# Performance work log

Hardware: AMD Instinct MI355X
Metric: run time of the kernel (lower is better)

## Reference

```python
import jax, jax.numpy as jnp
from jax import lax
import numpy as np

B = 8192
NUM_CTX = 300; NUM_STN = 300; NUM_GPE = 20; NUM_GPI = 2; NUM_OUT = 20
FF_DIM = 20; FF_STEPS = 20; STN_ITERS = 50
ETA_GPE = 1.0; ETA_STN = 1.0 / 3.0; ETA_GPI = 0.1
A1 = 1.0; A2 = 1.0; THETAD1 = 0.0; THETAD2 = 0.0
UNITS = (64, 128, 64)

_SPECS = [("vf0", UNITS[0], NUM_CTX), ("vf1", UNITS[1], UNITS[0]), ("vf2", UNITS[2], UNITS[1]), ("vf3", 1, UNITS[2]),
          ("jd1", FF_DIM, NUM_CTX), ("jd2", FF_DIM, NUM_CTX), ("kd1", FF_DIM, NUM_CTX), ("kd2", FF_DIM, NUM_CTX),
          ("sg", NUM_GPE, NUM_STN), ("gs", NUM_STN, NUM_GPE), ("glat", NUM_GPE, NUM_GPE), ("slat", NUM_STN, NUM_STN),
          ("d1gpi", NUM_GPI, FF_DIM), ("stngpi", NUM_GPI, NUM_STN),
          ("ih", 4 * NUM_OUT, NUM_GPI), ("hh", 4 * NUM_OUT, NUM_OUT)]


def _lin_init(k, out_d, in_d):
    kw, kb = jax.random.split(k)
    bound = 1.0 / np.sqrt(in_d)
    w = jax.random.uniform(kw, (out_d, in_d), minval=-bound, maxval=bound, dtype=jnp.float32)
    b = jax.random.uniform(kb, (out_d,), minval=-bound, maxval=bound, dtype=jnp.float32)
    return w, b


def setup_inputs() -> dict:
    key = jax.random.key(0)
    ks = iter(jax.random.split(key, 40))
    inp = {}
    inp["stimulus"] = jax.random.normal(next(ks), (B, NUM_CTX), dtype=jnp.float32)
    inp["deltavf"] = jax.random.normal(next(ks), (B, 1), dtype=jnp.float32)
    inp["hx0"] = jax.random.uniform(next(ks), (B, NUM_OUT), dtype=jnp.float32)
    inp["cx0"] = jax.random.uniform(next(ks), (B, NUM_OUT), dtype=jnp.float32)
    for name, o, i in _SPECS:
        w, b = _lin_init(next(ks), o, i)
        inp["w_" + name] = w
        inp["b_" + name] = b
    return inp


def _lin(x, w, b):
    return x @ w.T + b


def _lstm_cell(x, h, c, w_ih, b_ih, w_hh, b_hh):
    gates = _lin(x, w_ih, b_ih) + _lin(h, w_hh, b_hh)
    i, f, g, o = jnp.split(gates, 4, axis=-1)  # torch LSTMCell gate order
    c_new = jax.nn.sigmoid(f) * c + jax.nn.sigmoid(i) * jnp.tanh(g)
    h_new = jax.nn.sigmoid(o) * jnp.tanh(c_new)
    return h_new, c_new


def reference(stimulus, deltavf, hx0, cx0,
              w_vf0, b_vf0, w_vf1, b_vf1, w_vf2, b_vf2, w_vf3, b_vf3,
              w_jd1, b_jd1, w_jd2, b_jd2, w_kd1, b_kd1, w_kd2, b_kd2,
              w_sg, b_sg, w_gs, b_gs, w_glat, b_glat, w_slat, b_slat,
              w_d1gpi, b_d1gpi, w_stngpi, b_stngpi,
              w_ih, b_ih, w_hh, b_hh):
    bsz = stimulus.shape[0]
    # value function head
    h = jax.nn.relu(_lin(stimulus, w_vf0, b_vf0))
    h = jax.nn.relu(_lin(h, w_vf1, b_vf1))
    h = jax.nn.relu(_lin(h, w_vf2, b_vf2))
    vt = jnp.tanh(_lin(h, w_vf3, b_vf3))  # [B, 1]

    lamd1 = jax.nn.sigmoid(A1 * (deltavf - THETAD1))  # [B, 1]
    lamd2 = jax.nn.sigmoid(A2 * (deltavf - THETAD2))  # [B, 1]

    # loop-invariant striatal drives (computed every iter in torch, same value)
    J_D1 = _lin(stimulus, w_jd1, b_jd1)
    J_D2 = _lin(stimulus, w_jd2, b_jd2)
    K_D1 = _lin(stimulus, w_kd1, b_kd1)
    K_D2 = _lin(stimulus, w_kd2, b_kd2)

    def ff_step(carry, _):
        v1, v2 = carry
        v1 = jax.nn.sigmoid(lamd1 * (J_D1 * (1.0 - v1) + (1.0 - K_D1) * v1))
        v2 = jax.nn.sigmoid(lamd2 * (J_D2 * (1.0 - v2) + (1.0 - K_D2) * v2))
        return (v1, v2), None

    z_ff = jnp.zeros((bsz, FF_DIM), dtype=stimulus.dtype)
    (V_D1, V_D2), _ = lax.scan(ff_step, (z_ff, z_ff), None, length=FF_STEPS)

    V_GPi_DP = _lin(V_D1, w_d1gpi, b_d1gpi)  # [B, num_gpi]

    def stn_step(carry, _):
        xgpe, xstn, vstn, vgpi, hx, cx = carry
        xgpe = xgpe + ETA_GPE * (-xgpe + _lin(vstn, w_sg, b_sg) + _lin(xgpe, w_glat, b_glat) - V_D2)
        xstn = xstn + ETA_STN * (-xstn + _lin(xgpe, w_gs, b_gs) + _lin(vstn, w_slat, b_slat))
        vstn = jnp.tanh(lamd2 * xstn)
        V_GPi_IP = lamd2 * _lin(vstn, w_stngpi, b_stngpi)
        vgpi = vgpi + ETA_GPI * (-vgpi - V_GPi_DP + 2.0 * V_GPi_IP)
        hx, cx = _lstm_cell(-vgpi, hx, cx, w_ih, b_ih, w_hh, b_hh)
        return (xgpe, xstn, vstn, vgpi, hx, cx), None

    carry0 = (jnp.zeros((bsz, NUM_GPE), dtype=stimulus.dtype),
              jnp.zeros((bsz, NUM_STN), dtype=stimulus.dtype),
              jnp.zeros((bsz, NUM_STN), dtype=stimulus.dtype),  # tanh(lamd2*0) = 0
              jnp.zeros((bsz, NUM_GPI), dtype=stimulus.dtype),
              hx0, cx0)
    carry, _ = lax.scan(stn_step, carry0, None, length=STN_ITERS)
    hx = carry[4]
    return hx, vt
```

## Files before the change

kernel.cpp:

```cpp
#include <hip/hip_runtime.h>


typedef _Float16 f16_t;
typedef _Float16 f16x8 __attribute__((ext_vector_type(8)));
typedef _Float16 f16x4 __attribute__((ext_vector_type(4)));
typedef float floatx4 __attribute__((ext_vector_type(4)));

#define BTOT 8192
#define BM   32
#define NTHR 512
#define NBLK 256
#define VSTR 328
#define XST  32

struct Params {
  const float *stimulus, *deltavf, *hx0, *cx0;
  const float *w_vf0, *b_vf0, *w_vf1, *b_vf1, *w_vf2, *b_vf2, *w_vf3, *b_vf3;
  const float *w_jd1, *b_jd1, *w_jd2, *b_jd2, *w_kd1, *b_kd1, *w_kd2, *b_kd2;
  const float *w_sg, *b_sg, *w_gs, *b_gs, *w_glat, *b_glat, *w_slat, *b_slat;
  const float *w_d1gpi, *b_d1gpi, *w_stngpi, *b_stngpi;
  const float *w_ih, *b_ih, *w_hh, *b_hh;
  float* out;
};

struct __align__(16) Smem {
  f16_t vstn[BM * VSTR];
  f16_t xgpe[2][BM * XST];
  f16_t hxf[BM * XST];
  f16_t wB2[21 * 512];
  f16_t wsp[10 * 512];
  f16_t whh[5 * 512];
  union { float h1f[BM * 128]; float scr[3200]; float gates[BM * 80]; } u;
  float h0f[BM * 64];
  float V_D2f[BM * 20];
  float bsumS[304];
  float bsg[20];
  float bihh[80], wih0[80], wih1[80];
  float DPs[BM * 2], vgpis[BM * 2], lamS[BM];
};

__device__ __forceinline__ float rcp_f(float x) { return __builtin_amdgcn_rcpf(x); }
__device__ __forceinline__ float sigm_fast(float x) { return rcp_f(1.f + __expf(-x)); }
__device__ __forceinline__ float tanh_fast(float x) { return 1.f - 2.f * rcp_f(1.f + __expf(2.f * x)); }

__device__ __forceinline__ f16x8 ldfrag(const float* row, int k0, int kmax, bool valid) {
  float4 z = make_float4(0.f, 0.f, 0.f, 0.f);
  int nv = valid ? (kmax - k0) : 0;
  float4 f0 = (nv >= 4) ? *(const float4*)(row + k0) : z;
  float4 f1 = (nv >= 8) ? *(const float4*)(row + k0 + 4) : z;
  f16x8 r;
  r[0] = (f16_t)f0.x; r[1] = (f16_t)f0.y; r[2] = (f16_t)f0.z; r[3] = (f16_t)f0.w;
  r[4] = (f16_t)f1.x; r[5] = (f16_t)f1.y; r[6] = (f16_t)f1.z; r[7] = (f16_t)f1.w;
  return r;
}

__global__ __launch_bounds__(NTHR, 2) void bg_main(Params P) {
  __shared__ Smem S;
  const int tid  = threadIdx.x;
  const int lane = tid & 63;
  const int wv   = tid >> 6;
  const int q    = lane >> 4;
  const int cl   = lane & 15;
  const int row0 = blockIdx.x * BM;
  const floatx4 zf = {0.f, 0.f, 0.f, 0.f};

  if (tid < BM) S.lamS[tid] = sigm_fast(P.deltavf[row0 + tid]);
  for (int i = tid; i < BM * 2; i += NTHR) S.vgpis[i] = 0.f;
  for (int i = tid; i < 2 * BM * XST; i += NTHR) ((f16_t*)S.xgpe)[i] = (f16_t)0.f;
  for (int i = tid; i < BM * XST; i += NTHR) {
    int m = i >> 5, j = i & 31;
    S.hxf[i] = (j < 20) ? (f16_t)P.hx0[row0 * 20 + m * 20 + j] : (f16_t)0.f;
  }
  for (int i = tid; i < BM * VSTR; i += NTHR) S.vstn[i] = (f16_t)0.f;
  for (int i = tid; i < 21 * 512; i += NTHR) {
    int t = i >> 9, l = (i >> 3) & 63, jj = i & 7;
    int c2 = l & 15, k = ((l >> 4) << 3) + jj;
    float v = 0.f;
    if (t < 19) { int n = t * 16 + c2; if (n < 300 && k < 20) v = P.w_gs[n * 20 + k]; }
    else        { int g = (t - 19) * 16 + c2; if (g < 20 && k < 20) v = P.w_glat[g * 20 + k]; }
    S.wB2[i] = (f16_t)v;
  }
  for (int i = tid; i < 10 * 512; i += NTHR) {
    int c = i >> 9, l = (i >> 3) & 63, jj = i & 7;
    int p = l & 15, k = c * 32 + ((l >> 4) << 3) + jj;
    float v = (p < 2 && k < 300) ? P.w_stngpi[p * 300 + k] : 0.f;
    S.wsp[i] = (f16_t)v;
  }
  for (int i = tid; i < 5 * 512; i += NTHR) {
    int t = i >> 9, l = (i >> 3) & 63, jj = i & 7;
    int g = t * 16 + (l & 15), k = ((l >> 4) << 3) + jj;
    S.whh[i] = (f16_t)((k < 20) ? P.w_hh[g * 20 + k] : 0.f);
  }
  for (int i = tid; i < 304; i += NTHR) S.bsumS[i] = (i < 300) ? (P.b_slat[i] + P.b_gs[i]) : 0.f;
  for (int i = tid; i < 20; i += NTHR)  S.bsg[i] = P.b_sg[i] + P.b_glat[i];
  for (int i = tid; i < 80; i += NTHR) {
    S.bihh[i] = P.b_ih[i] + P.b_hh[i];
    S.wih0[i] = P.w_ih[i * 2 + 0];
    S.wih1[i] = P.w_ih[i * 2 + 1];
  }

  {
    int o = tid & 63, mb = (tid >> 6) * 4;
    const float4* wr = (const float4*)(P.w_vf0 + o * 300);
    float bias = P.b_vf0[o], a[4];
#pragma unroll
    for (int u = 0; u < 4; ++u) a[u] = bias;
    for (int kq = 0; kq < 75; ++kq) {
      float4 w = wr[kq];
#pragma unroll
      for (int u = 0; u < 4; ++u) {
        float4 v = *(const float4*)(P.stimulus + (size_t)(row0 + mb + u) * 300 + kq * 4);
        a[u] = fmaf(v.x, w.x, a[u]); a[u] = fmaf(v.y, w.y, a[u]);
        a[u] = fmaf(v.z, w.z, a[u]); a[u] = fmaf(v.w, w.w, a[u]);
      }
    }
#pragma unroll
    for (int u = 0; u < 4; ++u) S.h0f[(mb + u) * 64 + o] = fmaxf(a[u], 0.f);
  }
  __syncthreads();
  {
    int o = tid & 127, mb = (tid >> 7) * 8;
    const float* wr = P.w_vf1 + o * 64;
    float bias = P.b_vf1[o], a[8];
#pragma unroll
    for (int u = 0; u < 8; ++u) a[u] = bias;
    for (int k = 0; k < 64; ++k) {
      float w = wr[k];
#pragma unroll
      for (int u = 0; u < 8; ++u) a[u] = fmaf(S.h0f[(mb + u) * 64 + k], w, a[u]);
    }
#pragma unroll
    for (int u = 0; u < 8; ++u) S.u.h1f[(mb + u) * 128 + o] = fmaxf(a[u], 0.f);
  }
  __syncthreads();
  {
    int o = tid & 63, mb = (tid >> 6) * 4;
    const float* wr = P.w_vf2 + o * 128;
    float bias = P.b_vf2[o], a[4];
#pragma unroll
    for (int u = 0; u < 4; ++u) a[u] = bias;
    for (int k = 0; k < 128; ++k) {
      float w = wr[k];
#pragma unroll
      for (int u = 0; u < 4; ++u) a[u] = fmaf(S.u.h1f[(mb + u) * 128 + k], w, a[u]);
    }
#pragma unroll
    for (int u = 0; u < 4; ++u) S.h0f[(mb + u) * 64 + o] = fmaxf(a[u], 0.f);
  }
  __syncthreads();
  {
    int oid = tid & 127, mb = (tid >> 7) * 8;
    if (oid < 80) {
      int which = oid / 20, o = oid - which * 20;
      const float *wp, *bp;
      if (which == 0)      { wp = P.w_jd1; bp = P.b_jd1; }
      else if (which == 1) { wp = P.w_jd2; bp = P.b_jd2; }
      else if (which == 2) { wp = P.w_kd1; bp = P.b_kd1; }
      else                 { wp = P.w_kd2; bp = P.b_kd2; }
      float bias = bp[o], a[8];
#pragma unroll
      for (int u = 0; u < 8; ++u) a[u] = bias;
      for (int kq = 0; kq < 75; ++kq) {
        float4 w = *(const float4*)(wp + o * 300 + kq * 4);
#pragma unroll
        for (int u = 0; u < 8; ++u) {
          float4 v = *(const float4*)(P.stimulus + (size_t)(row0 + mb + u) * 300 + kq * 4);
          a[u] = fmaf(v.x, w.x, a[u]); a[u] = fmaf(v.y, w.y, a[u]);
          a[u] = fmaf(v.z, w.z, a[u]); a[u] = fmaf(v.w, w.w, a[u]);
        }
      }
#pragma unroll
      for (int u = 0; u < 8; ++u) S.u.scr[which * 640 + (mb + u) * 20 + o] = a[u];
    }
    if (tid < BM) {
      float a = P.b_vf3[0];
      for (int k = 0; k < 64; ++k) a = fmaf(S.h0f[tid * 64 + k], P.w_vf3[k], a);
      P.out[(size_t)BTOT * 20 + row0 + tid] = tanh_fast(a);
    }
  }
  __syncthreads();
  for (int i = tid; i < BM * 20; i += NTHR) {
    int m = i / 20;
    float j1 = S.u.scr[i],        j2 = S.u.scr[640 + i];
    float k1 = S.u.scr[1280 + i], k2 = S.u.scr[1920 + i];
    float L = S.lamS[m], v1 = 0.f, v2 = 0.f;
    for (int s = 0; s < 20; ++s) {
      v1 = sigm_fast(L * (j1 * (1.f - v1) + (1.f - k1) * v1));
      v2 = sigm_fast(L * (j2 * (1.f - v2) + (1.f - k2) * v2));
    }
    S.u.scr[2560 + i] = v1;
    S.V_D2f[i] = v2;
  }
  __syncthreads();
  if (tid < BM * 2) {
    int m = tid >> 1, p2 = tid & 1;
    float a = P.b_d1gpi[p2];
    for (int o = 0; o < 20; ++o) a = fmaf(S.u.scr[2560 + m * 20 + o], P.w_d1gpi[p2 * 20 + o], a);
    S.DPs[tid] = a;
  }
  __syncthreads();

  f16x8 Ws[3][10];
#pragma unroll
  for (int j = 0; j < 3; ++j) {
    int t = wv + 8 * j;
    if (t < 19) {
      int n = t * 16 + cl;
#pragma unroll
      for (int c = 0; c < 10; ++c)
        Ws[j][c] = ldfrag(P.w_slat + (size_t)(n < 300 ? n : 0) * 300, c * 32 + q * 8, 300, n < 300);
    } else if (t < 21) {
      int g = (t - 19) * 16 + cl;
#pragma unroll
      for (int c = 0; c < 10; ++c)
        Ws[j][c] = ldfrag(P.w_sg + (size_t)(g < 20 ? g : 0) * 300, c * 32 + q * 8, 300, g < 20);
    } else {
      f16x8 z;
#pragma unroll
      for (int e = 0; e < 8; ++e) z[e] = (f16_t)0.f;
#pragma unroll
      for (int c = 0; c < 10; ++c) Ws[j][c] = z;
    }
  }
  const float lam0 = S.lamS[cl], lam1 = S.lamS[cl + 16];
  const float bstn0 = P.b_stngpi[0], bstn1 = P.b_stngpi[1];
  const int e0 = tid,        m0 = e0 / 20, j0 = e0 - m0 * 20;
  const int e1 = tid + NTHR, m1 = e1 / 20, j1 = e1 - m1 * 20;
  const bool hase1 = (tid < BM * 20 - NTHR);
  float cxr0 = P.cx0[row0 * 20 + e0], hxr0 = P.hx0[row0 * 20 + e0];
  float cxr1 = hase1 ? P.cx0[row0 * 20 + e1] : 0.f;
  float hxr1 = hase1 ? P.hx0[row0 * 20 + e1] : 0.f;

  float xs[3][2][4];
#pragma unroll
  for (int j = 0; j < 3; ++j)
#pragma unroll
    for (int mf = 0; mf < 2; ++mf)
#pragma unroll
      for (int r = 0; r < 4; ++r) xs[j][mf][r] = 0.f;

  for (int it = 0; it < 50; ++it) {
    const int po = it & 1, pn = po ^ 1;
    floatx4 acc[3][2];
#pragma unroll
    for (int j = 0; j < 3; ++j) { acc[j][0] = zf; acc[j][1] = zf; }

#pragma unroll
    for (int c = 0; c < 10; ++c) {
      f16x8 b0 = *(const f16x8*)&S.vstn[cl * VSTR + c * 32 + q * 8];
      f16x8 b1 = *(const f16x8*)&S.vstn[(16 + cl) * VSTR + c * 32 + q * 8];
#pragma unroll
      for (int j = 0; j < 3; ++j) {
        if (wv + 8 * j < 21) {
          acc[j][0] = __builtin_amdgcn_mfma_f32_16x16x32_f16(Ws[j][c], b0, acc[j][0], 0, 0, 0);
          acc[j][1] = __builtin_amdgcn_mfma_f32_16x16x32_f16(Ws[j][c], b1, acc[j][1], 0, 0, 0);
        }
      }
    }
    if (wv == 3 || wv == 4) {
      f16x8 Wg = *(const f16x8*)&S.wB2[(wv + 16) * 512 + lane * 8];
      f16x8 g0 = *(const f16x8*)&S.xgpe[po][cl * XST + q * 8];
      f16x8 g1 = *(const f16x8*)&S.xgpe[po][(16 + cl) * XST + q * 8];
      acc[2][0] = __builtin_amdgcn_mfma_f32_16x16x32_f16(Wg, g0, acc[2][0], 0, 0, 0);
      acc[2][1] = __builtin_amdgcn_mfma_f32_16x16x32_f16(Wg, g1, acc[2][1], 0, 0, 0);
      int g0i = (wv - 3) * 16 + q * 4;
      if (g0i < 20) {
        floatx4 bg4 = *(const floatx4*)&S.bsg[g0i];
#pragma unroll
        for (int mf = 0; mf < 2; ++mf) {
          int batch = cl + 16 * mf;
          floatx4 vd4 = *(const floatx4*)&S.V_D2f[batch * 20 + g0i];
          f16x4 pk;
#pragma unroll
          for (int r = 0; r < 4; ++r) pk[r] = (f16_t)(acc[2][mf][r] + bg4[r] - vd4[r]);
          *(f16x4*)&S.xgpe[pn][batch * XST + g0i] = pk;
        }
      }
    }
    __syncthreads();

    {
      f16x8 x0 = *(const f16x8*)&S.xgpe[pn][cl * XST + q * 8];
      f16x8 x1 = *(const f16x8*)&S.xgpe[pn][(16 + cl) * XST + q * 8];
#pragma unroll
      for (int j = 0; j < 3; ++j) {
        int t = wv + 8 * j;
        if (t < 19) {
          f16x8 Wg = *(const f16x8*)&S.wB2[t * 512 + lane * 8];
          acc[j][0] = __builtin_amdgcn_mfma_f32_16x16x32_f16(Wg, x0, acc[j][0], 0, 0, 0);
          acc[j][1] = __builtin_amdgcn_mfma_f32_16x16x32_f16(Wg, x1, acc[j][1], 0, 0, 0);
        }
      }
#pragma unroll
      for (int j = 0; j < 3; ++j) {
        int t = wv + 8 * j;
        if (t < 19) {
          int n0 = t * 16 + q * 4;
          if (!(t == 18 && q == 3)) {
            floatx4 bs4 = *(const floatx4*)&S.bsumS[n0];
#pragma unroll
            for (int mf = 0; mf < 2; ++mf) {
              float lm = mf ? lam1 : lam0;
              f16x4 pk;
#pragma unroll
              for (int r = 0; r < 4; ++r) {
                float xo = xs[j][mf][r];
                float xn = xo + (1.0f / 3.0f) * (acc[j][mf][r] + bs4[r] - xo);
                xs[j][mf][r] = xn;
                pk[r] = (f16_t)tanh_fast(lm * xn);
              }
              *(f16x4*)&S.vstn[(cl + 16 * mf) * VSTR + n0] = pk;
            }
          }
        }
      }
    }
    __syncthreads();

    if (wv == 5) {
      floatx4 ip0 = zf, ip1 = zf;
#pragma unroll
      for (int c = 0; c < 10; ++c) {
        f16x8 Wp = *(const f16x8*)&S.wsp[c * 512 + lane * 8];
        f16x8 b0 = *(const f16x8*)&S.vstn[cl * VSTR + c * 32 + q * 8];
        f16x8 b1 = *(const f16x8*)&S.vstn[(16 + cl) * VSTR + c * 32 + q * 8];
        ip0 = __builtin_amdgcn_mfma_f32_16x16x32_f16(Wp, b0, ip0, 0, 0, 0);
        ip1 = __builtin_amdgcn_mfma_f32_16x16x32_f16(Wp, b1, ip1, 0, 0, 0);
      }
      if (q == 0) {
#pragma unroll
        for (int mf = 0; mf < 2; ++mf) {
          int batch = cl + 16 * mf;
          float lm = mf ? lam1 : lam0;
#pragma unroll
          for (int p = 0; p < 2; ++p) {
            float raw = (mf ? ip1[p] : ip0[p]) + (p ? bstn1 : bstn0);
            float ipv = lm * raw;
            int idx = batch * 2 + p;
            float v = S.vgpis[idx];
            v = v + 0.1f * (-v - S.DPs[idx] + 2.f * ipv);
            S.vgpis[idx] = v;
          }
        }
      }
    } else if (wv < 5) {
      f16x8 Wh = *(const f16x8*)&S.whh[wv * 512 + lane * 8];
      f16x8 h0 = *(const f16x8*)&S.hxf[cl * XST + q * 8];
      f16x8 h1 = *(const f16x8*)&S.hxf[(16 + cl) * XST + q * 8];
      floatx4 gA = __builtin_amdgcn_mfma_f32_16x16x32_f16(Wh, h0, zf, 0, 0, 0);
      floatx4 gB = __builtin_amdgcn_mfma_f32_16x16x32_f16(Wh, h1, zf, 0, 0, 0);
      int gb = wv * 16 + q * 4;
      *(floatx4*)&S.u.gates[cl * 80 + gb] = gA;
      *(floatx4*)&S.u.gates[(cl + 16) * 80 + gb] = gB;
    }
    __syncthreads();

    {
      float v0 = S.vgpis[m0 * 2], v1 = S.vgpis[m0 * 2 + 1];
      float gi = S.u.gates[m0 * 80 + j0]      + S.bihh[j0]      - S.wih0[j0] * v0      - S.wih1[j0] * v1;
      float gf = S.u.gates[m0 * 80 + 20 + j0] + S.bihh[20 + j0] - S.wih0[20 + j0] * v0 - S.wih1[20 + j0] * v1;
      float gg = S.u.gates[m0 * 80 + 40 + j0] + S.bihh[40 + j0] - S.wih0[40 + j0] * v0 - S.wih1[40 + j0] * v1;
      float go = S.u.gates[m0 * 80 + 60 + j0] + S.bihh[60 + j0] - S.wih0[60 + j0] * v0 - S.wih1[60 + j0] * v1;
      float cn = sigm_fast(gf) * cxr0 + sigm_fast(gi) * tanh_fast(gg);
      cxr0 = cn;
      hxr0 = sigm_fast(go) * tanh_fast(cn);
      S.hxf[m0 * XST + j0] = (f16_t)hxr0;
    }
    if (hase1) {
      float v0 = S.vgpis[m1 * 2], v1 = S.vgpis[m1 * 2 + 1];
      float gi = S.u.gates[m1 * 80 + j1]      + S.bihh[j1]      - S.wih0[j1] * v0      - S.wih1[j1] * v1;
      float gf = S.u.gates[m1 * 80 + 20 + j1] + S.bihh[20 + j1] - S.wih0[20 + j1] * v0 - S.wih1[20 + j1] * v1;
      float gg = S.u.gates[m1 * 80 + 40 + j1] + S.bihh[40 + j1] - S.wih0[40 + j1] * v0 - S.wih1[40 + j1] * v1;
      float go = S.u.gates[m1 * 80 + 60 + j1] + S.bihh[60 + j1] - S.wih0[60 + j1] * v0 - S.wih1[60 + j1] * v1;
      float cn = sigm_fast(gf) * cxr1 + sigm_fast(gi) * tanh_fast(gg);
      cxr1 = cn;
      hxr1 = sigm_fast(go) * tanh_fast(cn);
      S.hxf[m1 * XST + j1] = (f16_t)hxr1;
    }
    __syncthreads();
  }

  P.out[(size_t)row0 * 20 + e0] = hxr0;
  if (hase1) P.out[(size_t)row0 * 20 + e1] = hxr1;
}

extern "C" void kernel_launch(void* const* d_in, const int* in_sizes, int n_in,
                              void* d_out, int out_size, void* d_ws, size_t ws_size,
                              hipStream_t stream) {
  (void)in_sizes; (void)n_in; (void)out_size; (void)d_ws; (void)ws_size;
  Params P;
  P.stimulus = (const float*)d_in[0];
  P.deltavf  = (const float*)d_in[1];
  P.hx0 = (const float*)d_in[2];
  P.cx0 = (const float*)d_in[3];
  P.w_vf0 = (const float*)d_in[4];  P.b_vf0 = (const float*)d_in[5];
  P.w_vf1 = (const float*)d_in[6];  P.b_vf1 = (const float*)d_in[7];
  P.w_vf2 = (const float*)d_in[8];  P.b_vf2 = (const float*)d_in[9];
  P.w_vf3 = (const float*)d_in[10]; P.b_vf3 = (const float*)d_in[11];
  P.w_jd1 = (const float*)d_in[12]; P.b_jd1 = (const float*)d_in[13];
  P.w_jd2 = (const float*)d_in[14]; P.b_jd2 = (const float*)d_in[15];
  P.w_kd1 = (const float*)d_in[16]; P.b_kd1 = (const float*)d_in[17];
  P.w_kd2 = (const float*)d_in[18]; P.b_kd2 = (const float*)d_in[19];
  P.w_sg  = (const float*)d_in[20]; P.b_sg  = (const float*)d_in[21];
  P.w_gs  = (const float*)d_in[22]; P.b_gs  = (const float*)d_in[23];
  P.w_glat= (const float*)d_in[24]; P.b_glat= (const float*)d_in[25];
  P.w_slat= (const float*)d_in[26]; P.b_slat= (const float*)d_in[27];
  P.w_d1gpi  = (const float*)d_in[28]; P.b_d1gpi  = (const float*)d_in[29];
  P.w_stngpi = (const float*)d_in[30]; P.b_stngpi = (const float*)d_in[31];
  P.w_ih = (const float*)d_in[32]; P.b_ih = (const float*)d_in[33];
  P.w_hh = (const float*)d_in[34]; P.b_hh = (const float*)d_in[35];
  P.out  = (float*)d_out;
  bg_main<<<NBLK, NTHR, 0, stream>>>(P);
}
```

Before: 410.5 us.

## Pipeline GPi/LSTM stage on dedicated wavefront, overlapping next STN iteration

Gives the STN/GPe matrix products to seven wavefronts and hands the GPi readout plus the LSTM update to wavefront 7. That wavefront processes iteration it-1 while the others compute iteration it, which removes two of the four barriers per iteration. The stngpi and hh weights now live in that wave's registers instead of shared memory, LSTM state moves to shared arrays, and the h1 activations are stored as fp16 to shrink shared memory. The risks are serialising the LSTM work on a single wave and the lower precision of the h1 activations.

```diff
diff --git a/kernel.cpp b/kernel.cpp
--- a/kernel.cpp
+++ b/kernel.cpp
@@ -28,11 +28,14 @@
   f16_t xgpe[2][BM * XST];
   f16_t hxf[BM * XST];
   f16_t wB2[21 * 512];
-  f16_t wsp[10 * 512];
-  f16_t whh[5 * 512];
-  union { float h1f[BM * 128]; float scr[3200]; float gates[BM * 80]; } u;
+  union {
+    f16_t h1f[BM * 128];
+    float scr[2560];
+    float gates[BM * 80];
+  } u;
   float h0f[BM * 64];
   float V_D2f[BM * 20];
+  float cxL[BM * 20], hxL[BM * 20];
   float bsumS[304];
   float bsg[20];
   float bihh[80], wih0[80], wih1[80];
@@ -66,12 +69,16 @@
 
   if (tid < BM) S.lamS[tid] = sigm_fast(P.deltavf[row0 + tid]);
   for (int i = tid; i < BM * 2; i += NTHR) S.vgpis[i] = 0.f;
+  for (int i = tid; i < BM * VSTR; i += NTHR) S.vstn[i] = (f16_t)0.f;
   for (int i = tid; i < 2 * BM * XST; i += NTHR) ((f16_t*)S.xgpe)[i] = (f16_t)0.f;
   for (int i = tid; i < BM * XST; i += NTHR) {
     int m = i >> 5, j = i & 31;
     S.hxf[i] = (j < 20) ? (f16_t)P.hx0[row0 * 20 + m * 20 + j] : (f16_t)0.f;
   }
-  for (int i = tid; i < BM * VSTR; i += NTHR) S.vstn[i] = (f16_t)0.f;
+  for (int i = tid; i < BM * 20; i += NTHR) {
+    S.cxL[i] = P.cx0[row0 * 20 + i];
+    S.hxL[i] = P.hx0[row0 * 20 + i];
+  }
   for (int i = tid; i < 21 * 512; i += NTHR) {
     int t = i >> 9, l = (i >> 3) & 63, jj = i & 7;
     int c2 = l & 15, k = ((l >> 4) << 3) + jj;
@@ -80,17 +87,6 @@
     else        { int g = (t - 19) * 16 + c2; if (g < 20 && k < 20) v = P.w_glat[g * 20 + k]; }
     S.wB2[i] = (f16_t)v;
   }
-  for (int i = tid; i < 10 * 512; i += NTHR) {
-    int c = i >> 9, l = (i >> 3) & 63, jj = i & 7;
-    int p = l & 15, k = c * 32 + ((l >> 4) << 3) + jj;
-    float v = (p < 2 && k < 300) ? P.w_stngpi[p * 300 + k] : 0.f;
-    S.wsp[i] = (f16_t)v;
-  }
-  for (int i = tid; i < 5 * 512; i += NTHR) {
-    int t = i >> 9, l = (i >> 3) & 63, jj = i & 7;
-    int g = t * 16 + (l & 15), k = ((l >> 4) << 3) + jj;
-    S.whh[i] = (f16_t)((k < 20) ? P.w_hh[g * 20 + k] : 0.f);
-  }
   for (int i = tid; i < 304; i += NTHR) S.bsumS[i] = (i < 300) ? (P.b_slat[i] + P.b_gs[i]) : 0.f;
   for (int i = tid; i < 20; i += NTHR)  S.bsg[i] = P.b_sg[i] + P.b_glat[i];
   for (int i = tid; i < 80; i += NTHR) {
@@ -104,18 +100,18 @@
     const float4* wr = (const float4*)(P.w_vf0 + o * 300);
     float bias = P.b_vf0[o], a[4];
 #pragma unroll
-    for (int u = 0; u < 4; ++u) a[u] = bias;
+    for (int u2 = 0; u2 < 4; ++u2) a[u2] = bias;
     for (int kq = 0; kq < 75; ++kq) {
       float4 w = wr[kq];
 #pragma unroll
-      for (int u = 0; u < 4; ++u) {
-        float4 v = *(const float4*)(P.stimulus + (size_t)(row0 + mb + u) * 300 + kq * 4);
-        a[u] = fmaf(v.x, w.x, a[u]); a[u] = fmaf(v.y, w.y, a[u]);
-        a[u] = fmaf(v.z, w.z, a[u]); a[u] = fmaf(v.w, w.w, a[u]);
-      }
-    }
-#pragma unroll
-    for (int u = 0; u < 4; ++u) S.h0f[(mb + u) * 64 + o] = fmaxf(a[u], 0.f);
+      for (int u2 = 0; u2 < 4; ++u2) {
+        float4 v = *(const float4*)(P.stimulus + (size_t)(row0 + mb + u2) * 300 + kq * 4);
+        a[u2] = fmaf(v.x, w.x, a[u2]); a[u2] = fmaf(v.y, w.y, a[u2]);
+        a[u2] = fmaf(v.z, w.z, a[u2]); a[u2] = fmaf(v.w, w.w, a[u2]);
+      }
+    }
+#pragma unroll
+    for (int u2 = 0; u2 < 4; ++u2) S.h0f[(mb + u2) * 64 + o] = fmaxf(a[u2], 0.f);
   }
   __syncthreads();
   {
@@ -123,14 +119,14 @@
     const float* wr = P.w_vf1 + o * 64;
     float bias = P.b_vf1[o], a[8];
 #pragma unroll
-    for (int u = 0; u < 8; ++u) a[u] = bias;
+    for (int u2 = 0; u2 < 8; ++u2) a[u2] = bias;
     for (int k = 0; k < 64; ++k) {
       float w = wr[k];
 #pragma unroll
-      for (int u = 0; u < 8; ++u) a[u] = fmaf(S.h0f[(mb + u) * 64 + k], w, a[u]);
-    }
-#pragma unroll
-    for (int u = 0; u < 8; ++u) S.u.h1f[(mb + u) * 128 + o] = fmaxf(a[u], 0.f);
+      for (int u2 = 0; u2 < 8; ++u2) a[u2] = fmaf(S.h0f[(mb + u2) * 64 + k], w, a[u2]);
+    }
+#pragma unroll
+    for (int u2 = 0; u2 < 8; ++u2) S.u.h1f[(mb + u2) * 128 + o] = (f16_t)fmaxf(a[u2], 0.f);
   }
   __syncthreads();
   {
@@ -138,14 +134,14 @@
     const float* wr = P.w_vf2 + o * 128;
     float bias = P.b_vf2[o], a[4];
 #pragma unroll
-    for (int u = 0; u < 4; ++u) a[u] = bias;
+    for (int u2 = 0; u2 < 4; ++u2) a[u2] = bias;
     for (int k = 0; k < 128; ++k) {
       float w = wr[k];
 #pragma unroll
-      for (int u = 0; u < 4; ++u) a[u] = fmaf(S.u.h1f[(mb + u) * 128 + k], w, a[u]);
-    }
-#pragma unroll
-    for (int u = 0; u < 4; ++u) S.h0f[(mb + u) * 64 + o] = fmaxf(a[u], 0.f);
+      for (int u2 = 0; u2 < 4; ++u2) a[u2] = fmaf((float)S.u.h1f[(mb + u2) * 128 + k], w, a[u2]);
+    }
+#pragma unroll
+    for (int u2 = 0; u2 < 4; ++u2) S.h0f[(mb + u2) * 64 + o] = fmaxf(a[u2], 0.f);
   }
   __syncthreads();
   {
@@ -159,18 +155,18 @@
       else                 { wp = P.w_kd2; bp = P.b_kd2; }
       float bias = bp[o], a[8];
 #pragma unroll
-      for (int u = 0; u < 8; ++u) a[u] = bias;
+      for (int u2 = 0; u2 < 8; ++u2) a[u2] = bias;
       for (int kq = 0; kq < 75; ++kq) {
         float4 w = *(const float4*)(wp + o * 300 + kq * 4);
 #pragma unroll
-        for (int u = 0; u < 8; ++u) {
-          float4 v = *(const float4*)(P.stimulus + (size_t)(row0 + mb + u) * 300 + kq * 4);
-          a[u] = fmaf(v.x, w.x, a[u]); a[u] = fmaf(v.y, w.y, a[u]);
-          a[u] = fmaf(v.z, w.z, a[u]); a[u] = fmaf(v.w, w.w, a[u]);
+        for (int u2 = 0; u2 < 8; ++u2) {
+          float4 v = *(const float4*)(P.stimulus + (size_t)(row0 + mb + u2) * 300 + kq * 4);
+          a[u2] = fmaf(v.x, w.x, a[u2]); a[u2] = fmaf(v.y, w.y, a[u2]);
+          a[u2] = fmaf(v.z, w.z, a[u2]); a[u2] = fmaf(v.w, w.w, a[u2]);
         }
       }
 #pragma unroll
-      for (int u = 0; u < 8; ++u) S.u.scr[which * 640 + (mb + u) * 20 + o] = a[u];
+      for (int u2 = 0; u2 < 8; ++u2) S.u.scr[which * 640 + (mb + u2) * 20 + o] = a[u2];
     }
     if (tid < BM) {
       float a = P.b_vf3[0];
@@ -188,48 +184,47 @@
       v1 = sigm_fast(L * (j1 * (1.f - v1) + (1.f - k1) * v1));
       v2 = sigm_fast(L * (j2 * (1.f - v2) + (1.f - k2) * v2));
     }
-    S.u.scr[2560 + i] = v1;
     S.V_D2f[i] = v2;
+    S.h0f[i] = v1;
   }
   __syncthreads();
   if (tid < BM * 2) {
     int m = tid >> 1, p2 = tid & 1;
     float a = P.b_d1gpi[p2];
-    for (int o = 0; o < 20; ++o) a = fmaf(S.u.scr[2560 + m * 20 + o], P.w_d1gpi[p2 * 20 + o], a);
+    for (int o = 0; o < 20; ++o) a = fmaf(S.h0f[m * 20 + o], P.w_d1gpi[p2 * 20 + o], a);
     S.DPs[tid] = a;
   }
   __syncthreads();
 
   f16x8 Ws[3][10];
-#pragma unroll
-  for (int j = 0; j < 3; ++j) {
-    int t = wv + 8 * j;
-    if (t < 19) {
-      int n = t * 16 + cl;
-#pragma unroll
-      for (int c = 0; c < 10; ++c)
-        Ws[j][c] = ldfrag(P.w_slat + (size_t)(n < 300 ? n : 0) * 300, c * 32 + q * 8, 300, n < 300);
-    } else if (t < 21) {
-      int g = (t - 19) * 16 + cl;
-#pragma unroll
-      for (int c = 0; c < 10; ++c)
-        Ws[j][c] = ldfrag(P.w_sg + (size_t)(g < 20 ? g : 0) * 300, c * 32 + q * 8, 300, g < 20);
-    } else {
-      f16x8 z;
-#pragma unroll
-      for (int e = 0; e < 8; ++e) z[e] = (f16_t)0.f;
-#pragma unroll
-      for (int c = 0; c < 10; ++c) Ws[j][c] = z;
-    }
-  }
-  const float lam0 = S.lamS[cl], lam1 = S.lamS[cl + 16];
-  const float bstn0 = P.b_stngpi[0], bstn1 = P.b_stngpi[1];
-  const int e0 = tid,        m0 = e0 / 20, j0 = e0 - m0 * 20;
-  const int e1 = tid + NTHR, m1 = e1 / 20, j1 = e1 - m1 * 20;
-  const bool hase1 = (tid < BM * 20 - NTHR);
-  float cxr0 = P.cx0[row0 * 20 + e0], hxr0 = P.hx0[row0 * 20 + e0];
-  float cxr1 = hase1 ? P.cx0[row0 * 20 + e1] : 0.f;
-  float hxr1 = hase1 ? P.hx0[row0 * 20 + e1] : 0.f;
+  if (wv < 7) {
+#pragma unroll
+    for (int j = 0; j < 3; ++j) {
+      int t = wv + 7 * j;
+      if (t < 19) {
+        int n = t * 16 + cl;
+#pragma unroll
+        for (int c = 0; c < 10; ++c)
+          Ws[j][c] = ldfrag(P.w_slat + (size_t)(n < 300 ? n : 0) * 300, c * 32 + q * 8, 300, n < 300);
+      } else {
+        int g = (t - 19) * 16 + cl;
+#pragma unroll
+        for (int c = 0; c < 10; ++c)
+          Ws[j][c] = ldfrag(P.w_sg + (size_t)(g < 20 ? g : 0) * 300, c * 32 + q * 8, 300, g < 20);
+      }
+    }
+  }
+  f16x8 Wsp[10], Whh[5];
+  float bstn0 = 0.f, bstn1 = 0.f;
+  if (wv == 7) {
+#pragma unroll
+    for (int c = 0; c < 10; ++c)
+      Wsp[c] = ldfrag(P.w_stngpi + (size_t)(cl < 2 ? cl : 0) * 300, c * 32 + q * 8, 300, cl < 2);
+#pragma unroll
+    for (int gt = 0; gt < 5; ++gt)
+      Whh[gt] = ldfrag(P.w_hh + (size_t)(gt * 16 + cl) * 20, q * 8, 20, true);
+    bstn0 = P.b_stngpi[0]; bstn1 = P.b_stngpi[1];
+  }
 
   float xs[3][2][4];
 #pragma unroll
@@ -238,6 +233,68 @@
     for (int mf = 0; mf < 2; ++mf)
 #pragma unroll
       for (int r = 0; r < 4; ++r) xs[j][mf][r] = 0.f;
+
+  const int cm = lane >> 1, cj0 = (lane & 1) * 10;
+
+  auto consume = [&]() {
+    floatx4 ip0 = zf, ip1 = zf;
+#pragma unroll
+    for (int c = 0; c < 10; ++c) {
+      f16x8 b0 = *(const f16x8*)&S.vstn[cl * VSTR + c * 32 + q * 8];
+      f16x8 b1 = *(const f16x8*)&S.vstn[(16 + cl) * VSTR + c * 32 + q * 8];
+      ip0 = __builtin_amdgcn_mfma_f32_16x16x32_f16(Wsp[c], b0, ip0, 0, 0, 0);
+      ip1 = __builtin_amdgcn_mfma_f32_16x16x32_f16(Wsp[c], b1, ip1, 0, 0, 0);
+    }
+    if (q == 0) {
+#pragma unroll
+      for (int mf = 0; mf < 2; ++mf) {
+        int batch = cl + 16 * mf;
+        float lm = S.lamS[batch];
+#pragma unroll
+        for (int p = 0; p < 2; ++p) {
+          float raw = (mf ? ip1[p] : ip0[p]) + (p ? bstn1 : bstn0);
+          int idx = batch * 2 + p;
+          float v = S.vgpis[idx];
+          v = v + 0.1f * (-v - S.DPs[idx] + 2.f * (lm * raw));
+          S.vgpis[idx] = v;
+        }
+      }
+    }
+    f16x8 h0 = *(const f16x8*)&S.hxf[cl * XST + q * 8];
+    f16x8 h1 = *(const f16x8*)&S.hxf[(16 + cl) * XST + q * 8];
+    float vA0 = S.vgpis[cl * 2], vA1 = S.vgpis[cl * 2 + 1];
+    float vB0 = S.vgpis[(cl + 16) * 2], vB1 = S.vgpis[(cl + 16) * 2 + 1];
+#pragma unroll
+    for (int gt = 0; gt < 5; ++gt) {
+      floatx4 gA = __builtin_amdgcn_mfma_f32_16x16x32_f16(Whh[gt], h0, zf, 0, 0, 0);
+      floatx4 gB = __builtin_amdgcn_mfma_f32_16x16x32_f16(Whh[gt], h1, zf, 0, 0, 0);
+      int gb = gt * 16 + q * 4;
+      floatx4 bi = *(const floatx4*)&S.bihh[gb];
+      floatx4 w0 = *(const floatx4*)&S.wih0[gb];
+      floatx4 w1 = *(const floatx4*)&S.wih1[gb];
+#pragma unroll
+      for (int r = 0; r < 4; ++r) {
+        gA[r] += bi[r] - w0[r] * vA0 - w1[r] * vA1;
+        gB[r] += bi[r] - w0[r] * vB0 - w1[r] * vB1;
+      }
+      *(floatx4*)&S.u.gates[cl * 80 + gb] = gA;
+      *(floatx4*)&S.u.gates[(cl + 16) * 80 + gb] = gB;
+    }
+#pragma unroll
+    for (int u2 = 0; u2 < 10; ++u2) {
+      int j = cj0 + u2;
+      float gi = S.u.gates[cm * 80 + j];
+      float gf = S.u.gates[cm * 80 + 20 + j];
+      float gg = S.u.gates[cm * 80 + 40 + j];
+      float go = S.u.gates[cm * 80 + 60 + j];
+      float cx = S.cxL[cm * 20 + j];
+      float cn = sigm_fast(gf) * cx + sigm_fast(gi) * tanh_fast(gg);
+      S.cxL[cm * 20 + j] = cn;
+      float hn = sigm_fast(go) * tanh_fast(cn);
+      S.hxL[cm * 20 + j] = hn;
+      S.hxf[cm * XST + j] = (f16_t)hn;
+    }
+  };
 
   for (int it = 0; it < 50; ++it) {
     const int po = it & 1, pn = po ^ 1;
@@ -245,62 +302,58 @@
 #pragma unroll
     for (int j = 0; j < 3; ++j) { acc[j][0] = zf; acc[j][1] = zf; }
 
-#pragma unroll
-    for (int c = 0; c < 10; ++c) {
-      f16x8 b0 = *(const f16x8*)&S.vstn[cl * VSTR + c * 32 + q * 8];
-      f16x8 b1 = *(const f16x8*)&S.vstn[(16 + cl) * VSTR + c * 32 + q * 8];
-#pragma unroll
-      for (int j = 0; j < 3; ++j) {
-        if (wv + 8 * j < 21) {
+    if (wv < 7) {
+#pragma unroll
+      for (int c = 0; c < 10; ++c) {
+        f16x8 b0 = *(const f16x8*)&S.vstn[cl * VSTR + c * 32 + q * 8];
+        f16x8 b1 = *(const f16x8*)&S.vstn[(16 + cl) * VSTR + c * 32 + q * 8];
+#pragma unroll
+        for (int j = 0; j < 3; ++j) {
           acc[j][0] = __builtin_amdgcn_mfma_f32_16x16x32_f16(Ws[j][c], b0, acc[j][0], 0, 0, 0);
           acc[j][1] = __builtin_amdgcn_mfma_f32_16x16x32_f16(Ws[j][c], b1, acc[j][1], 0, 0, 0);
         }
       }
-    }
-    if (wv == 3 || wv == 4) {
-      f16x8 Wg = *(const f16x8*)&S.wB2[(wv + 16) * 512 + lane * 8];
-      f16x8 g0 = *(const f16x8*)&S.xgpe[po][cl * XST + q * 8];
-      f16x8 g1 = *(const f16x8*)&S.xgpe[po][(16 + cl) * XST + q * 8];
-      acc[2][0] = __builtin_amdgcn_mfma_f32_16x16x32_f16(Wg, g0, acc[2][0], 0, 0, 0);
-      acc[2][1] = __builtin_amdgcn_mfma_f32_16x16x32_f16(Wg, g1, acc[2][1], 0, 0, 0);
-      int g0i = (wv - 3) * 16 + q * 4;
-      if (g0i < 20) {
-        floatx4 bg4 = *(const floatx4*)&S.bsg[g0i];
-#pragma unroll
-        for (int mf = 0; mf < 2; ++mf) {
-          int batch = cl + 16 * mf;
-          floatx4 vd4 = *(const floatx4*)&S.V_D2f[batch * 20 + g0i];
-          f16x4 pk;
-#pragma unroll
-          for (int r = 0; r < 4; ++r) pk[r] = (f16_t)(acc[2][mf][r] + bg4[r] - vd4[r]);
-          *(f16x4*)&S.xgpe[pn][batch * XST + g0i] = pk;
+      if (wv >= 5) {
+        f16x8 Wg = *(const f16x8*)&S.wB2[(wv + 14) * 512 + lane * 8];
+        f16x8 g0 = *(const f16x8*)&S.xgpe[po][cl * XST + q * 8];
+        f16x8 g1 = *(const f16x8*)&S.xgpe[po][(16 + cl) * XST + q * 8];
+        acc[2][0] = __builtin_amdgcn_mfma_f32_16x16x32_f16(Wg, g0, acc[2][0], 0, 0, 0);
+        acc[2][1] = __builtin_amdgcn_mfma_f32_16x16x32_f16(Wg, g1, acc[2][1], 0, 0, 0);
+        int g0i = (wv - 5) * 16 + q * 4;
+        if (g0i < 20) {
+          floatx4 bg4 = *(const floatx4*)&S.bsg[g0i];
+#pragma unroll
+          for (int mf = 0; mf < 2; ++mf) {
+            int batch = cl + 16 * mf;
+            floatx4 vd4 = *(const floatx4*)&S.V_D2f[batch * 20 + g0i];
+            f16x4 pk;
+#pragma unroll
+            for (int r = 0; r < 4; ++r) pk[r] = (f16_t)(acc[2][mf][r] + bg4[r] - vd4[r]);
+            *(f16x4*)&S.xgpe[pn][batch * XST + g0i] = pk;
+          }
         }
       }
+    } else if (it > 0) {
+      consume();
     }
     __syncthreads();
 
-    {
+    if (wv < 7) {
       f16x8 x0 = *(const f16x8*)&S.xgpe[pn][cl * XST + q * 8];
       f16x8 x1 = *(const f16x8*)&S.xgpe[pn][(16 + cl) * XST + q * 8];
 #pragma unroll
       for (int j = 0; j < 3; ++j) {
-        int t = wv + 8 * j;
+        int t = wv + 7 * j;
         if (t < 19) {
           f16x8 Wg = *(const f16x8*)&S.wB2[t * 512 + lane * 8];
           acc[j][0] = __builtin_amdgcn_mfma_f32_16x16x32_f16(Wg, x0, acc[j][0], 0, 0, 0);
           acc[j][1] = __builtin_amdgcn_mfma_f32_16x16x32_f16(Wg, x1, acc[j][1], 0, 0, 0);
-        }
-      }
-#pragma unroll
-      for (int j = 0; j < 3; ++j) {
-        int t = wv + 8 * j;
-        if (t < 19) {
           int n0 = t * 16 + q * 4;
           if (!(t == 18 && q == 3)) {
             floatx4 bs4 = *(const floatx4*)&S.bsumS[n0];
 #pragma unroll
             for (int mf = 0; mf < 2; ++mf) {
-              float lm = mf ? lam1 : lam0;
+              float lm = S.lamS[cl + 16 * mf];
               f16x4 pk;
 #pragma unroll
               for (int r = 0; r < 4; ++r) {
@@ -316,72 +369,14 @@
       }
     }
     __syncthreads();
-
-    if (wv == 5) {
-      floatx4 ip0 = zf, ip1 = zf;
-#pragma unroll
-      for (int c = 0; c < 10; ++c) {
-        f16x8 Wp = *(const f16x8*)&S.wsp[c * 512 + lane * 8];
-        f16x8 b0 = *(const f16x8*)&S.vstn[cl * VSTR + c * 32 + q * 8];
-        f16x8 b1 = *(const f16x8*)&S.vstn[(16 + cl) * VSTR + c * 32 + q * 8];
-        ip0 = __builtin_amdgcn_mfma_f32_16x16x32_f16(Wp, b0, ip0, 0, 0, 0);
-        ip1 = __builtin_amdgcn_mfma_f32_16x16x32_f16(Wp, b1, ip1, 0, 0, 0);
-      }
-      if (q == 0) {
-#pragma unroll
-        for (int mf = 0; mf < 2; ++mf) {
-          int batch = cl + 16 * mf;
-          float lm = mf ? lam1 : lam0;
-#pragma unroll
-          for (int p = 0; p < 2; ++p) {
-            float raw = (mf ? ip1[p] : ip0[p]) + (p ? bstn1 : bstn0);
-            float ipv = lm * raw;
-            int idx = batch * 2 + p;
-            float v = S.vgpis[idx];
-            v = v + 0.1f * (-v - S.DPs[idx] + 2.f * ipv);
-            S.vgpis[idx] = v;
-          }
-        }
-      }
-    } else if (wv < 5) {
-      f16x8 Wh = *(const f16x8*)&S.whh[wv * 512 + lane * 8];
-      f16x8 h0 = *(const f16x8*)&S.hxf[cl * XST + q * 8];
-      f16x8 h1 = *(const f16x8*)&S.hxf[(16 + cl) * XST + q * 8];
-      floatx4 gA = __builtin_amdgcn_mfma_f32_16x16x32_f16(Wh, h0, zf, 0, 0, 0);
-      floatx4 gB = __builtin_amdgcn_mfma_f32_16x16x32_f16(Wh, h1, zf, 0, 0, 0);
-      int gb = wv * 16 + q * 4;
-      *(floatx4*)&S.u.gates[cl * 80 + gb] = gA;
-      *(floatx4*)&S.u.gates[(cl + 16) * 80 + gb] = gB;
-    }
-    __syncthreads();
-
-    {
-      float v0 = S.vgpis[m0 * 2], v1 = S.vgpis[m0 * 2 + 1];
-      float gi = S.u.gates[m0 * 80 + j0]      + S.bihh[j0]      - S.wih0[j0] * v0      - S.wih1[j0] * v1;
-      float gf = S.u.gates[m0 * 80 + 20 + j0] + S.bihh[20 + j0] - S.wih0[20 + j0] * v0 - S.wih1[20 + j0] * v1;
-      float gg = S.u.gates[m0 * 80 + 40 + j0] + S.bihh[40 + j0] - S.wih0[40 + j0] * v0 - S.wih1[40 + j0] * v1;
-      float go = S.u.gates[m0 * 80 + 60 + j0] + S.bihh[60 + j0] - S.wih0[60 + j0] * v0 - S.wih1[60 + j0] * v1;
-      float cn = sigm_fast(gf) * cxr0 + sigm_fast(gi) * tanh_fast(gg);
-      cxr0 = cn;
-      hxr0 = sigm_fast(go) * tanh_fast(cn);
-      S.hxf[m0 * XST + j0] = (f16_t)hxr0;
-    }
-    if (hase1) {
-      float v0 = S.vgpis[m1 * 2], v1 = S.vgpis[m1 * 2 + 1];
-      float gi = S.u.gates[m1 * 80 + j1]      + S.bihh[j1]      - S.wih0[j1] * v0      - S.wih1[j1] * v1;
-      float gf = S.u.gates[m1 * 80 + 20 + j1] + S.bihh[20 + j1] - S.wih0[20 + j1] * v0 - S.wih1[20 + j1] * v1;
-      float gg = S.u.gates[m1 * 80 + 40 + j1] + S.bihh[40 + j1] - S.wih0[40 + j1] * v0 - S.wih1[40 + j1] * v1;
-      float go = S.u.gates[m1 * 80 + 60 + j1] + S.bihh[60 + j1] - S.wih0[60 + j1] * v0 - S.wih1[60 + j1] * v1;
-      float cn = sigm_fast(gf) * cxr1 + sigm_fast(gi) * tanh_fast(gg);
-      cxr1 = cn;
-      hxr1 = sigm_fast(go) * tanh_fast(cn);
-      S.hxf[m1 * XST + j1] = (f16_t)hxr1;
-    }
-    __syncthreads();
-  }
-
-  P.out[(size_t)row0 * 20 + e0] = hxr0;
-  if (hase1) P.out[(size_t)row0 * 20 + e1] = hxr1;
+  }
+
+  if (wv == 7) {
+    consume();
+#pragma unroll
+    for (int u2 = 0; u2 < 10; ++u2)
+      P.out[(size_t)row0 * 20 + cm * 20 + cj0 + u2] = S.hxL[cm * 20 + cj0 + u2];
+  }
 }
 
 extern "C" void kernel_launch(void* const* d_in, const int* in_sizes, int n_in,
```

Result: slower. 544.2 us (+32.6%).
